# Optimization experiments

Hardware: AMD Instinct MI355X
Metric: run time of the kernel (lower is better)

The kernel has to match this reference:

```python
import jax, jax.numpy as jnp
import numpy as np

N_TOK, D_MODEL, N_EXPERTS, TOP_K = 8192, 512, 8, 2


def setup_inputs() -> dict:
    key = jax.random.key(0)
    k1, k2, k3 = jax.random.split(key, 3)
    x = jax.random.normal(k1, (N_TOK, D_MODEL), jnp.float32)
    w_gate = jax.random.normal(k2, (D_MODEL, N_EXPERTS), jnp.float32) * 0.02
    expert_w = jax.random.normal(k3, (N_EXPERTS, D_MODEL, D_MODEL), jnp.float32) * (D_MODEL ** -0.5)
    return {"x": x, "w_gate": w_gate, "expert_w": expert_w, "top_k": TOP_K}


def _cv_sq(v):
    m = jnp.mean(v)
    return jnp.var(v) / (m * m + 1e-10)


def reference(x, w_gate, expert_w, top_k):
    # ---- Gate (clean top-k gating, eval mode of noisy-top-k) ----
    logits = x @ w_gate                              # [N, E]
    top_vals, top_idx = jax.lax.top_k(logits, top_k)  # [N, k]
    top_gates = jax.nn.softmax(top_vals, axis=-1)
    n, e = logits.shape
    gates = jnp.zeros((n, e), x.dtype).at[jnp.arange(n)[:, None], top_idx].set(top_gates)

    # ---- dispatch -> per-expert GEMM -> log-domain combine ----
    # combine(): stitched = cat(expert_out).exp() * nonzero_gates; index_add over
    # batch index; zeros -> eps; log. Dense-equivalent (tokens with gate 0
    # contribute exactly nothing):
    expert_out = jnp.einsum('nd,edf->nef', x, expert_w)   # per-expert outputs [N, E, D]
    combined = jnp.einsum('ne,nef->nf', gates, jnp.exp(expert_out))  # [N, D]
    eps = np.float32(np.finfo(np.float64).eps)
    combined = jnp.where(combined == 0, eps, combined)
    out = jnp.log(combined)

    # ---- load-balance aux loss: cv^2(importance) + cv^2(load) ----
    importance = gates.sum(0)
    load = (gates > 0).sum(0).astype(x.dtype)
    balance_loss = _cv_sq(importance) + _cv_sq(load)
    return out, balance_loss
```

## Files before the change

kernel.cpp:

```cpp
#include <hip/hip_runtime.h>
#include <hip/hip_bf16.h>
#include <math.h>

#define N_TOK 8192
#define D 512
#define NE 8

typedef float f32x4 __attribute__((ext_vector_type(4)));
typedef __bf16 bf16x8 __attribute__((ext_vector_type(8)));
typedef unsigned short u16;
typedef u16 u16x8 __attribute__((ext_vector_type(8)));

#define OFF_TOKE  256
#define OFF_TOKG  65792
#define OFF_BUCK  131328
#define OFF_XB    (1u << 20)
#define OFF_EWT   (OFF_XB + 8u * 1024 * 1024)
#define OFF_Y     (OFF_EWT + 4u * 1024 * 1024)

__device__ __forceinline__ u16 f2b(float v) {
    __hip_bfloat16 h = __float2bfloat16(v);
    return *reinterpret_cast<u16*>(&h);
}
__device__ __forceinline__ float b2f(u16 u) {
    __hip_bfloat16 h;
    *reinterpret_cast<u16*>(&h) = u;
    return __bfloat162float(h);
}

typedef __attribute__((address_space(1))) const void* gp1_t;
typedef __attribute__((address_space(3))) void* lp3_t;
__device__ __forceinline__ void gload16(const void* g, void* l) {
    __builtin_amdgcn_global_load_lds((gp1_t)g, (lp3_t)l, 16, 0, 0);
}

__global__ __launch_bounds__(256) void gate_prep_kernel(
    const float* __restrict__ x, const float* __restrict__ wg,
    const float* __restrict__ ew,
    int* __restrict__ tok_e, float* __restrict__ tok_g, u16* __restrict__ xb,
    u16* __restrict__ ewt)
{
    __shared__ __align__(16) float sbuf[64 * 65];
    int b = blockIdx.x;
    int tid = threadIdx.x;

    if (b >= 2048) {
        int pb = b - 2048;
        float (*tile)[65] = (float(*)[65])sbuf;
        int e = pb >> 6, dt = (pb >> 3) & 7, ftl = pb & 7;
        int c = tid & 63, rq = tid >> 6;
        const float* src = ew + (size_t)e * D * D + (size_t)(dt * 64) * D + ftl * 64;
#pragma unroll
        for (int i = 0; i < 16; ++i) {
            int r = i * 4 + rq;
            tile[r][c] = src[(size_t)r * D + c];
        }
        __syncthreads();
        u16* dst = ewt + (size_t)e * D * D + (size_t)(ftl * 64) * D + dt * 64;
#pragma unroll
        for (int i = 0; i < 16; ++i) {
            int f = i * 4 + rq;
            dst[(size_t)f * D + c] = f2b(tile[c][f]);
        }
        return;
    }

    float* wgs = sbuf;
    for (int i = tid; i < NE * D; i += 256) {
        int d = i >> 3, e = i & 7;
        wgs[e * D + d] = wg[i];
    }
    __syncthreads();

    int wave = tid >> 6, lane = tid & 63;
    int n = b * 4 + wave;
    const float* xr = x + (size_t)n * D;
    u16* xbr = xb + (size_t)n * D;

    float p[NE];
#pragma unroll
    for (int e = 0; e < NE; ++e) p[e] = 0.f;
#pragma unroll
    for (int it = 0; it < 8; ++it) {
        float xv = xr[it * 64 + lane];
        xbr[it * 64 + lane] = f2b(xv);
#pragma unroll
        for (int e = 0; e < NE; ++e)
            p[e] += xv * wgs[e * D + it * 64 + lane];
    }
#pragma unroll
    for (int off = 32; off > 0; off >>= 1) {
#pragma unroll
        for (int e = 0; e < NE; ++e)
            p[e] += __shfl_xor(p[e], off);
    }

    if (lane == 0) {
        int e1 = 0; float v1 = p[0];
#pragma unroll
        for (int e = 1; e < NE; ++e) if (p[e] > v1) { v1 = p[e]; e1 = e; }
        int e2 = -1; float v2 = -INFINITY;
#pragma unroll
        for (int e = 0; e < NE; ++e) if (e != e1 && p[e] > v2) { v2 = p[e]; e2 = e; }
        float t = __expf(v2 - v1);
        float inv = 1.f / (1.f + t);
        tok_e[2 * n] = e1;     tok_e[2 * n + 1] = e2;
        tok_g[2 * n] = inv;    tok_g[2 * n + 1] = t * inv;
    }
}

__global__ __launch_bounds__(256) void bucketize_kernel(
    const int* __restrict__ tok_e, const float* __restrict__ tok_g,
    int* __restrict__ count, float* __restrict__ imp, int* __restrict__ bucket)
{
    __shared__ int lcnt[NE], lbase[NE];
    __shared__ float limp[NE];
    int tid = threadIdx.x;
    if (tid < NE) { lcnt[tid] = 0; limp[tid] = 0.f; }
    __syncthreads();

    int n = blockIdx.x * 256 + tid;
    int e1 = tok_e[2 * n], e2 = tok_e[2 * n + 1];
    float g1 = tok_g[2 * n], g2 = tok_g[2 * n + 1];
    int o1 = atomicAdd(&lcnt[e1], 1);
    int o2 = atomicAdd(&lcnt[e2], 1);
    atomicAdd(&limp[e1], g1);
    atomicAdd(&limp[e2], g2);
    __syncthreads();
    if (tid < NE) {
        lbase[tid] = atomicAdd(&count[tid], lcnt[tid]);
        atomicAdd(&imp[tid], limp[tid]);
    }
    __syncthreads();
    bucket[e1 * N_TOK + lbase[e1] + o1] = 2 * n;
    bucket[e2 * N_TOK + lbase[e2] + o2] = 2 * n + 1;
}

__global__ __launch_bounds__(256) void moe_gemm(
    const u16* __restrict__ xb, const u16* __restrict__ ewt,
    const int* __restrict__ count, const int* __restrict__ bucket,
    u16* __restrict__ y)
{
    int b = blockIdx.x;
    int ft = b & 3;
    int tt = (b >> 2) & 63;
    int e  = b >> 8;
    int cnt = count[e];
    if (tt * 128 >= cnt) return;

    __shared__ int sl[128];
    __shared__ __align__(16) u16 smem[16384];
    u16* As = smem;
    u16* Bs = smem + 8192;

    int tid = threadIdx.x;
    if (tid < 128) {
        int idx = tt * 128 + tid;
        sl[tid] = (idx < cnt) ? bucket[e * N_TOK + idx] : -1;
    }
    __syncthreads();

    int w = tid >> 6, l = tid & 63;
    int c8 = (l & 3) * 8;
    int r0 = w * 32 + (l >> 2);
    int r1 = r0 + 16;
    int s0 = sl[r0], s1 = sl[r1];
    int ta0 = (s0 < 0) ? 0 : (s0 >> 1);
    int ta1 = (s1 < 0) ? 0 : (s1 >> 1);
    const u16* gA0 = xb + (size_t)ta0 * D + c8;
    const u16* gA1 = xb + (size_t)ta1 * D + c8;
    const u16* gB0 = ewt + ((size_t)e * D + ft * 128 + r0) * D + c8;
    const u16* gB1 = ewt + ((size_t)e * D + ft * 128 + r1) * D + c8;
    u16* lA0 = &As[(w * 32) * 32];
    u16* lA1 = &As[(w * 32 + 16) * 32];
    u16* lB0 = &Bs[(w * 32) * 32];
    u16* lB1 = &Bs[(w * 32 + 16) * 32];

    int wm = w & 1, wn = w >> 1;
    int lm = l & 15, quad = l >> 4, kq = quad * 8;

    f32x4 acc[4][4] = {};

    for (int kc = 0; kc < 16; ++kc) {
        __syncthreads();
        gload16(gA0 + kc * 32, lA0);
        gload16(gA1 + kc * 32, lA1);
        gload16(gB0 + kc * 32, lB0);
        gload16(gB1 + kc * 32, lB1);
        __syncthreads();

        bf16x8 af[4], bfv[4];
#pragma unroll
        for (int i = 0; i < 4; ++i)
            af[i] = *(const bf16x8*)&As[(wm * 64 + i * 16 + lm) * 32 + kq];
#pragma unroll
        for (int j = 0; j < 4; ++j)
            bfv[j] = *(const bf16x8*)&Bs[(wn * 64 + j * 16 + lm) * 32 + kq];
#pragma unroll
        for (int i = 0; i < 4; ++i)
#pragma unroll
            for (int j = 0; j < 4; ++j)
                acc[i][j] = __builtin_amdgcn_mfma_f32_16x16x32_bf16(
                    af[i], bfv[j], acc[i][j], 0, 0, 0);
    }

    __syncthreads();
    u16* Es = smem + w * 2304;
#pragma unroll
    for (int h = 0; h < 2; ++h) {
#pragma unroll
        for (int i2 = 0; i2 < 2; ++i2) {
            int i = h * 2 + i2;
#pragma unroll
            for (int j = 0; j < 4; ++j)
#pragma unroll
                for (int r = 0; r < 4; ++r)
                    Es[(i2 * 16 + quad * 4 + r) * 72 + j * 16 + lm] =
                        f2b(acc[i][j][r]);
        }
        int row = l >> 1, hc = l & 1;
        int s = sl[wm * 64 + h * 32 + row];
        const u16* src = Es + row * 72 + hc * 32;
        u16* dst = y + (size_t)((s < 0) ? 0 : s) * D + ft * 128 + wn * 64 + hc * 32;
        if (s >= 0) {
#pragma unroll
            for (int c = 0; c < 4; ++c)
                *(u16x8*)(dst + c * 8) = *(const u16x8*)(src + c * 8);
        }
    }
}

__global__ __launch_bounds__(256) void combine_kernel(
    const u16* __restrict__ y, const float* __restrict__ tok_g,
    const int* __restrict__ count, const float* __restrict__ imp,
    float* __restrict__ out)
{
    if (blockIdx.x == 4096) {
        if (threadIdx.x == 0) {
            float mi = 0.f, ml = 0.f;
            for (int e = 0; e < NE; ++e) { mi += imp[e]; ml += (float)count[e]; }
            mi *= 0.125f; ml *= 0.125f;
            float vi = 0.f, vl = 0.f;
            for (int e = 0; e < NE; ++e) {
                float di = imp[e] - mi;          vi += di * di;
                float dl = (float)count[e] - ml; vl += dl * dl;
            }
            vi *= 0.125f; vl *= 0.125f;
            out[N_TOK * D] = vi / (mi * mi + 1e-10f) + vl / (ml * ml + 1e-10f);
        }
        return;
    }
    int idx = blockIdx.x * 256 + threadIdx.x;
    int n = idx >> 7;
    int c = (idx & 127) * 4;
    const ushort4 ua = *(const ushort4*)(y + (size_t)(2 * n) * D + c);
    const ushort4 ub = *(const ushort4*)(y + (size_t)(2 * n + 1) * D + c);
    float g1 = tok_g[2 * n], g2 = tok_g[2 * n + 1];
    const float eps = 2.2204460492503131e-16f;
    float4 r;
    float v;
    v = g1 * __expf(b2f(ua.x)) + g2 * __expf(b2f(ub.x)); r.x = __logf(v == 0.f ? eps : v);
    v = g1 * __expf(b2f(ua.y)) + g2 * __expf(b2f(ub.y)); r.y = __logf(v == 0.f ? eps : v);
    v = g1 * __expf(b2f(ua.z)) + g2 * __expf(b2f(ub.z)); r.z = __logf(v == 0.f ? eps : v);
    v = g1 * __expf(b2f(ua.w)) + g2 * __expf(b2f(ub.w)); r.w = __logf(v == 0.f ? eps : v);
    *(float4*)(out + (size_t)n * D + c) = r;
}

extern "C" void kernel_launch(void* const* d_in, const int* in_sizes, int n_in,
                              void* d_out, int out_size, void* d_ws, size_t ws_size,
                              hipStream_t stream)
{
    const float* x  = (const float*)d_in[0];
    const float* wg = (const float*)d_in[1];
    const float* ew = (const float*)d_in[2];
    char* ws = (char*)d_ws;
    int*   count  = (int*)(ws + 0);
    float* imp    = (float*)(ws + 64);
    int*   tok_e  = (int*)(ws + OFF_TOKE);
    float* tok_g  = (float*)(ws + OFF_TOKG);
    int*   bucket = (int*)(ws + OFF_BUCK);
    u16*   xb     = (u16*)(ws + OFF_XB);
    u16*   ewt    = (u16*)(ws + OFF_EWT);
    u16*   y      = (u16*)(ws + OFF_Y);
    float* out    = (float*)d_out;

    hipMemsetAsync(ws, 0, 128, stream);
    gate_prep_kernel<<<2048 + 512, 256, 0, stream>>>(x, wg, ew, tok_e, tok_g, xb, ewt);
    bucketize_kernel<<<N_TOK / 256, 256, 0, stream>>>(tok_e, tok_g, count, imp, bucket);
    moe_gemm<<<NE * 64 * 4, 256, 0, stream>>>(xb, ewt, count, bucket, y);
    combine_kernel<<<4097, 256, 0, stream>>>(y, tok_g, count, imp, out);
}
```

Before: 120.4 us.

## Double-buffer GEMM LDS tiles and widen combine kernel vector loads

The expert GEMM now uses two LDS buffers. The loads for the next K-chunk are issued before the MFMAs on the current chunk, which removes one barrier per iteration and overlaps global loads with compute. The combine kernel processes 8 bf16 elements per thread instead of 4, halving the grid and using 16-byte loads. The larger LDS footprint (about 64 KB per block) may cut occupancy.

```diff
diff --git a/kernel.cpp b/kernel.cpp
--- a/kernel.cpp
+++ b/kernel.cpp
@@ -149,9 +149,7 @@
     if (tt * 128 >= cnt) return;
 
     __shared__ int sl[128];
-    __shared__ __align__(16) u16 smem[16384];
-    u16* As = smem;
-    u16* Bs = smem + 8192;
+    __shared__ __align__(16) u16 smem[32768];
 
     int tid = threadIdx.x;
     if (tid < 128) {
@@ -171,23 +169,32 @@
     const u16* gA1 = xb + (size_t)ta1 * D + c8;
     const u16* gB0 = ewt + ((size_t)e * D + ft * 128 + r0) * D + c8;
     const u16* gB1 = ewt + ((size_t)e * D + ft * 128 + r1) * D + c8;
-    u16* lA0 = &As[(w * 32) * 32];
-    u16* lA1 = &As[(w * 32 + 16) * 32];
-    u16* lB0 = &Bs[(w * 32) * 32];
-    u16* lB1 = &Bs[(w * 32 + 16) * 32];
+    int wo = w * 1024;
 
     int wm = w & 1, wn = w >> 1;
     int lm = l & 15, quad = l >> 4, kq = quad * 8;
 
     f32x4 acc[4][4] = {};
 
+    {
+        u16* nb = smem;
+        gload16(gA0, nb + wo);
+        gload16(gA1, nb + wo + 512);
+        gload16(gB0, nb + 8192 + wo);
+        gload16(gB1, nb + 8192 + wo + 512);
+    }
+
     for (int kc = 0; kc < 16; ++kc) {
         __syncthreads();
-        gload16(gA0 + kc * 32, lA0);
-        gload16(gA1 + kc * 32, lA1);
-        gload16(gB0 + kc * 32, lB0);
-        gload16(gB1 + kc * 32, lB1);
-        __syncthreads();
+        if (kc < 15) {
+            u16* nb = smem + ((kc + 1) & 1) * 16384;
+            gload16(gA0 + (kc + 1) * 32, nb + wo);
+            gload16(gA1 + (kc + 1) * 32, nb + wo + 512);
+            gload16(gB0 + (kc + 1) * 32, nb + 8192 + wo);
+            gload16(gB1 + (kc + 1) * 32, nb + 8192 + wo + 512);
+        }
+        const u16* As = smem + (kc & 1) * 16384;
+        const u16* Bs = As + 8192;
 
         bf16x8 af[4], bfv[4];
 #pragma unroll
@@ -235,7 +242,7 @@
     const int* __restrict__ count, const float* __restrict__ imp,
     float* __restrict__ out)
 {
-    if (blockIdx.x == 4096) {
+    if (blockIdx.x == 2048) {
         if (threadIdx.x == 0) {
             float mi = 0.f, ml = 0.f;
             for (int e = 0; e < NE; ++e) { mi += imp[e]; ml += (float)count[e]; }
@@ -251,19 +258,21 @@
         return;
     }
     int idx = blockIdx.x * 256 + threadIdx.x;
-    int n = idx >> 7;
-    int c = (idx & 127) * 4;
-    const ushort4 ua = *(const ushort4*)(y + (size_t)(2 * n) * D + c);
-    const ushort4 ub = *(const ushort4*)(y + (size_t)(2 * n + 1) * D + c);
+    int n = idx >> 6;
+    int c = (idx & 63) * 8;
+    const u16x8 ua = *(const u16x8*)(y + (size_t)(2 * n) * D + c);
+    const u16x8 ub = *(const u16x8*)(y + (size_t)(2 * n + 1) * D + c);
     float g1 = tok_g[2 * n], g2 = tok_g[2 * n + 1];
     const float eps = 2.2204460492503131e-16f;
-    float4 r;
-    float v;
-    v = g1 * __expf(b2f(ua.x)) + g2 * __expf(b2f(ub.x)); r.x = __logf(v == 0.f ? eps : v);
-    v = g1 * __expf(b2f(ua.y)) + g2 * __expf(b2f(ub.y)); r.y = __logf(v == 0.f ? eps : v);
-    v = g1 * __expf(b2f(ua.z)) + g2 * __expf(b2f(ub.z)); r.z = __logf(v == 0.f ? eps : v);
-    v = g1 * __expf(b2f(ua.w)) + g2 * __expf(b2f(ub.w)); r.w = __logf(v == 0.f ? eps : v);
-    *(float4*)(out + (size_t)n * D + c) = r;
+    float r[8];
+#pragma unroll
+    for (int i = 0; i < 8; ++i) {
+        float v = g1 * __expf(b2f(ua[i])) + g2 * __expf(b2f(ub[i]));
+        r[i] = __logf(v == 0.f ? eps : v);
+    }
+    float* o = out + (size_t)n * D + c;
+    *(float4*)(o)     = *(float4*)&r[0];
+    *(float4*)(o + 4) = *(float4*)&r[4];
 }
 
 extern "C" void kernel_launch(void* const* d_in, const int* in_sizes, int n_in,
@@ -288,5 +297,5 @@
     gate_prep_kernel<<<2048 + 512, 256, 0, stream>>>(x, wg, ew, tok_e, tok_g, xb, ewt);
     bucketize_kernel<<<N_TOK / 256, 256, 0, stream>>>(tok_e, tok_g, count, imp, bucket);
     moe_gemm<<<NE * 64 * 4, 256, 0, stream>>>(xb, ewt, count, bucket, y);
-    combine_kernel<<<4097, 256, 0, stream>>>(y, tok_g, count, imp, out);
-}
+    combine_kernel<<<2049, 256, 0, stream>>>(y, tok_g, count, imp, out);
+}
```

Result: slower. 128.0 us (+6.3%).
